# Performance work log

Hardware: AMD Instinct MI355X
Metric: run time of the kernel (lower is better)

The kernel has to match this reference:

```python
import jax, jax.numpy as jnp
import numpy as np

NUM_HEADS = 16
HEAD_DIM = 64  # att_output_dim // num_heads = 1024 // 16


def setup_inputs() -> dict:
    key = jax.random.key(0)
    ks = jax.random.split(key, 7)
    B, S, D_IN, D_OUT = 4, 2048, 1024, 1024
    std = 1.0 / np.sqrt(D_IN)
    return {
        "ts10_input": jax.random.normal(ks[0], (B, S, D_IN), dtype=jnp.float32),
        "Wq": jax.random.uniform(ks[1], (D_IN, D_OUT), jnp.float32, -std, std),
        "bq": jax.random.uniform(ks[2], (D_OUT,), jnp.float32, -std, std),
        "Wk": jax.random.uniform(ks[3], (D_IN, D_OUT), jnp.float32, -std, std),
        "bk": jax.random.uniform(ks[4], (D_OUT,), jnp.float32, -std, std),
        "Wv": jax.random.uniform(ks[5], (D_IN, D_OUT), jnp.float32, -std, std),
        "bv": jax.random.uniform(ks[6], (D_OUT,), jnp.float32, -std, std),
        "mask": 1,
    }


def reference(ts10_input, Wq, bq, Wk, bk, Wv, bv, mask):
    B, S, _ = ts10_input.shape
    H, Dh = NUM_HEADS, HEAD_DIM

    def split_heads(x):  # (B,S,H*Dh) -> (B,H,S,Dh)
        return x.reshape(B, S, H, Dh).transpose(0, 2, 1, 3)

    q = split_heads(ts10_input @ Wq + bq)
    k = split_heads(ts10_input @ Wk + bk)
    v = split_heads(ts10_input @ Wv + bv)

    scores = jnp.einsum("bhqd,bhkd->bhqk", q, k) / jnp.sqrt(jnp.float32(Dh))
    if mask:
        causal = jnp.tril(jnp.ones((S, S), dtype=bool))  # keep lower triangle incl diag
        scores = jnp.where(causal, scores, -jnp.inf)
    probs = jax.nn.softmax(scores, axis=-1)
    ctx = jnp.einsum("bhqk,bhkd->bhqd", probs, v)
    return ctx.transpose(0, 2, 1, 3).reshape(B, S, H * Dh)
```

## Files before the change

kernel.cpp:

```cpp
#include <hip/hip_runtime.h>

typedef __bf16 bf16x8 __attribute__((ext_vector_type(8)));
typedef __bf16 bf16x4 __attribute__((ext_vector_type(4)));
typedef short s16x4 __attribute__((ext_vector_type(4)));
typedef float f32x4 __attribute__((ext_vector_type(4)));
typedef unsigned short u16x8 __attribute__((ext_vector_type(8)));
typedef unsigned short u16x4 __attribute__((ext_vector_type(4)));
typedef unsigned int u32x2 __attribute__((ext_vector_type(2)));
typedef unsigned int __attribute__((address_space(1))) as1_uint;
typedef unsigned int __attribute__((address_space(3))) as3_uint;

#define S_LEN 2048
#define NB 4
#define NH 16
#define HD 64
#define DM 1024

#define Q_SCALE 0.18033688011112042f

__device__ __forceinline__ unsigned short f2bf(float f) {
  union { float f; unsigned int u; } v; v.f = f;
  unsigned int r = v.u + 0x7fffu + ((v.u >> 16) & 1u);
  return (unsigned short)(r >> 16);
}

__device__ __forceinline__ unsigned int fbits(float f) {
  union { float f; unsigned int u; } v; v.f = f;
  return v.u;
}

__device__ __forceinline__ f32x4 mfma16(u16x4 a, u16x4 b, f32x4 c) {
#if __has_builtin(__builtin_amdgcn_mfma_f32_16x16x16_bf16)
  return __builtin_amdgcn_mfma_f32_16x16x16_bf16(
      __builtin_bit_cast(bf16x4, a), __builtin_bit_cast(bf16x4, b), c, 0, 0, 0);
#else
  return __builtin_amdgcn_mfma_f32_16x16x16bf16_1k(
      __builtin_bit_cast(s16x4, a), __builtin_bit_cast(s16x4, b), c, 0, 0, 0);
#endif
}

__global__ __launch_bounds__(256) void cvt_x(const float* __restrict__ x,
                                             unsigned short* __restrict__ xb) {
  int i = (blockIdx.x * 256 + threadIdx.x) * 8;
  f32x4 a = *(const f32x4*)(x + i);
  f32x4 b = *(const f32x4*)(x + i + 4);
  u16x8 o;
  o[0] = f2bf(a[0]); o[1] = f2bf(a[1]); o[2] = f2bf(a[2]); o[3] = f2bf(a[3]);
  o[4] = f2bf(b[0]); o[5] = f2bf(b[1]); o[6] = f2bf(b[2]); o[7] = f2bf(b[3]);
  *(u16x8*)(xb + i) = o;
}

__global__ __launch_bounds__(256) void cvt_wt(const float* __restrict__ Wq,
                                              const float* __restrict__ Wk,
                                              const float* __restrict__ Wv,
                                              unsigned short* __restrict__ wt) {
  const float* W = (blockIdx.z == 0) ? Wq : (blockIdx.z == 1) ? Wk : Wv;
  unsigned short* WT = wt + (size_t)blockIdx.z * DM * DM;
  __shared__ float tile[32][33];
  int tx = threadIdx.x & 31, ty = threadIdx.x >> 5;
  int k0 = blockIdx.x * 32, n0 = blockIdx.y * 32;
#pragma unroll
  for (int i = 0; i < 4; ++i)
    tile[ty + 8 * i][tx] = W[(size_t)(k0 + ty + 8 * i) * DM + n0 + tx];
  __syncthreads();
#pragma unroll
  for (int i = 0; i < 4; ++i)
    WT[(size_t)(n0 + ty + 8 * i) * DM + k0 + tx] = f2bf(tile[tx][ty + 8 * i]);
}

__global__ __launch_bounds__(256) void qkv_gemm(const unsigned short* __restrict__ xb,
                                                const unsigned short* __restrict__ wt,
                                                const float* __restrict__ bq,
                                                const float* __restrict__ bk,
                                                const float* __restrict__ bv,
                                                unsigned short* __restrict__ qo,
                                                unsigned short* __restrict__ ko,
                                                unsigned short* __restrict__ vto) {
  const int z = blockIdx.z;
  const unsigned short* WT = wt + (size_t)z * DM * DM;
  const float* bias = (z == 0) ? bq : (z == 1) ? bk : bv;
  const int m0 = blockIdx.x * 128;
  const int n0 = blockIdx.y * 128;
  __shared__ __align__(16) unsigned short Al[128 * 32];
  __shared__ __align__(16) unsigned short Bl[128 * 32];
  const int tid = threadIdx.x;
  const int wave = tid >> 6, lane = tid & 63, quad = lane >> 4, lw = lane & 15;
  const int wm = (wave >> 1) * 64, wn = (wave & 1) * 64;

  f32x4 acc[4][4];
#pragma unroll
  for (int mt = 0; mt < 4; ++mt)
#pragma unroll
    for (int nt = 0; nt < 4; ++nt) acc[mt][nt] = (f32x4){0.f, 0.f, 0.f, 0.f};

  for (int k0 = 0; k0 < DM; k0 += 32) {
    __syncthreads();
#pragma unroll
    for (int i = 0; i < 2; ++i) {
      int c = i * 256 + tid;
      const unsigned short* ga = xb + (size_t)(m0 + (c >> 2)) * DM + k0 + (c & 3) * 8;
      __builtin_amdgcn_global_load_lds((const as1_uint*)ga, (as3_uint*)(Al + c * 8), 16, 0, 0);
      const unsigned short* gb = WT + (size_t)(n0 + (c >> 2)) * DM + k0 + (c & 3) * 8;
      __builtin_amdgcn_global_load_lds((const as1_uint*)gb, (as3_uint*)(Bl + c * 8), 16, 0, 0);
    }
    __syncthreads();
    bf16x8 af[4], bfr[4];
#pragma unroll
    for (int mt = 0; mt < 4; ++mt)
      af[mt] = *(const bf16x8*)(Al + (wm + mt * 16 + lw) * 32 + quad * 8);
#pragma unroll
    for (int nt = 0; nt < 4; ++nt)
      bfr[nt] = *(const bf16x8*)(Bl + (wn + nt * 16 + lw) * 32 + quad * 8);
#pragma unroll
    for (int mt = 0; mt < 4; ++mt)
#pragma unroll
      for (int nt = 0; nt < 4; ++nt)
        acc[mt][nt] = __builtin_amdgcn_mfma_f32_16x16x32_bf16(af[mt], bfr[nt], acc[mt][nt], 0, 0, 0);
  }

  float bias4[4];
#pragma unroll
  for (int nt = 0; nt < 4; ++nt) bias4[nt] = bias[n0 + wn + nt * 16 + lw];

  if (z < 2) {
    unsigned short* dst = (z == 0) ? qo : ko;
    const float sc = (z == 0) ? Q_SCALE : 1.0f;
#pragma unroll
    for (int mt = 0; mt < 4; ++mt) {
#pragma unroll
      for (int nt = 0; nt < 4; ++nt) {
        int n = n0 + wn + nt * 16 + lw;
        int h = n >> 6, d = n & 63;
#pragma unroll
        for (int r = 0; r < 4; ++r) {
          int m = m0 + wm + mt * 16 + quad * 4 + r;
          int b = m >> 11, s = m & 2047;
          dst[((size_t)(b * NH + h) * S_LEN + s) * HD + d] = f2bf((acc[mt][nt][r] + bias4[nt]) * sc);
        }
      }
    }
  } else {
#pragma unroll
    for (int mt = 0; mt < 4; ++mt) {
#pragma unroll
      for (int nt = 0; nt < 4; ++nt) {
        int n = n0 + wn + nt * 16 + lw;
        int h = n >> 6, d = n & 63;
        int mb = m0 + wm + mt * 16 + quad * 4;
        int b = mb >> 11, s = mb & 2047;
        u16x4 pk;
#pragma unroll
        for (int r = 0; r < 4; ++r) pk[r] = f2bf(acc[mt][nt][r] + bias4[nt]);
        *(u16x4*)(vto + ((size_t)(b * NH + h) * HD + d) * S_LEN + s) = pk;
      }
    }
  }
}

__global__ __launch_bounds__(256, 4) void attn(const unsigned short* __restrict__ Qb,
                                               const unsigned short* __restrict__ Kb,
                                               const unsigned short* __restrict__ Vtb,
                                               float* __restrict__ out) {
  const int flat = blockIdx.x;
  const int bh_lo = flat & 7;
  const int qpair = (flat >> 3) & 15;
  const int bh_hi = flat >> 7;
  const int bh = bh_lo + 8 * bh_hi;
  const int b = bh >> 4, h = bh & 15;
  const int tid = threadIdx.x;
  const int wave = tid >> 6, lane = tid & 63;
  const int quad = lane >> 4, lw = lane & 15;
  const int qlo = qpair * 64;
  const int qhi = (31 - qpair) * 64;
  const unsigned short* Qp = Qb + (size_t)bh * S_LEN * HD;
  const unsigned short* Kp = Kb + (size_t)bh * S_LEN * HD;
  const unsigned short* Vp = Vtb + (size_t)bh * HD * S_LEN;

  __shared__ __align__(16) unsigned short Kl[64 * 64];
  __shared__ __align__(16) unsigned short Vl[64 * 64];

  bf16x8 aq[2][2];
#pragma unroll
  for (int rg = 0; rg < 2; ++rg) {
    const int qbase = rg ? qhi : qlo;
#pragma unroll
    for (int kc = 0; kc < 2; ++kc)
      aq[rg][kc] = *(const bf16x8*)(Qp + (size_t)(qbase + wave * 16 + lw) * HD + kc * 32 + quad * 8);
  }

  u16x4 ones4;
#pragma unroll
  for (int i = 0; i < 4; ++i) ones4[i] = 0x3F80;

  f32x4 accO[2][4];
  f32x4 accL[2];
#pragma unroll
  for (int rg = 0; rg < 2; ++rg) {
    accL[rg] = (f32x4){0.f, 0.f, 0.f, 0.f};
#pragma unroll
    for (int dg = 0; dg < 4; ++dg) accO[rg][dg] = (f32x4){0.f, 0.f, 0.f, 0.f};
  }

  const int qr0 = qlo + wave * 16 + lw;
  const int qr1 = qhi + wave * 16 + lw;

  const int T = 32 - qpair;
  for (int t = 0; t < T; ++t) {
    const int kv = t * 64;
    __syncthreads();
#pragma unroll
    for (int i = 0; i < 2; ++i) {
      int idx = i * 256 + tid;
      int r = idx >> 3, c = (idx & 7) ^ (r & 7);
      __builtin_amdgcn_global_load_lds((const as1_uint*)(Kp + (size_t)(kv + r) * HD + c * 8),
                                       (as3_uint*)(Kl + idx * 8), 16, 0, 0);
      __builtin_amdgcn_global_load_lds((const as1_uint*)(Vp + (size_t)r * S_LEN + kv + c * 8),
                                       (as3_uint*)(Vl + idx * 8), 16, 0, 0);
    }
    __syncthreads();

    const bool a0 = (t <= qpair);
    const bool d0 = (t == qpair);
    const bool d1 = (t == T - 1);

#pragma unroll
    for (int g = 0; g < 4; ++g) {
      const unsigned short* kp = Kl + (g * 16 + lw) * 64;
      const int sw = lw & 7;
      bf16x8 kf0 = *(const bf16x8*)(kp + ((quad ^ sw) * 8));
      bf16x8 kf1 = *(const bf16x8*)(kp + (((4 + quad) ^ sw) * 8));

      u16x4 pf[2];
#pragma unroll
      for (int rg = 0; rg < 2; ++rg) {
        if (rg == 0 && !a0) continue;
        f32x4 s = (f32x4){0.f, 0.f, 0.f, 0.f};
        s = __builtin_amdgcn_mfma_f32_16x16x32_bf16(kf0, aq[rg][0], s, 0, 0, 0);
        s = __builtin_amdgcn_mfma_f32_16x16x32_bf16(kf1, aq[rg][1], s, 0, 0, 0);
        const bool dg_ = rg ? d1 : d0;
        const int qr = rg ? qr1 : qr0;
        if (dg_) {
#pragma unroll
          for (int r = 0; r < 4; ++r) {
            float e = __builtin_amdgcn_exp2f(s[r]);
            s[r] = (kv + g * 16 + quad * 4 + r > qr) ? 0.f : e;
          }
        } else {
#pragma unroll
          for (int r = 0; r < 4; ++r) s[r] = __builtin_amdgcn_exp2f(s[r]);
        }
        u32x2 pk;
        pk[0] = (fbits(s[1]) & 0xFFFF0000u) | (fbits(s[0]) >> 16);
        pk[1] = (fbits(s[3]) & 0xFFFF0000u) | (fbits(s[2]) >> 16);
        pf[rg] = __builtin_bit_cast(u16x4, pk);
      }

#pragma unroll
      for (int dg = 0; dg < 4; ++dg) {
        const int row = dg * 16 + lw;
        const int slot = (2 * g + (quad >> 1)) ^ (lw & 7);
        u16x4 vf = *(const u16x4*)(Vl + row * 64 + slot * 8 + (quad & 1) * 4);
        if (a0) accO[0][dg] = mfma16(pf[0], vf, accO[0][dg]);
        accO[1][dg] = mfma16(pf[1], vf, accO[1][dg]);
      }
      if (a0) accL[0] = mfma16(pf[0], ones4, accL[0]);
      accL[1] = mfma16(pf[1], ones4, accL[1]);
    }
  }

#pragma unroll
  for (int rg = 0; rg < 2; ++rg) {
    const int qbase = rg ? qhi : qlo;
    float* op = out + ((size_t)b * S_LEN + qbase + wave * 16 + quad * 4) * DM + h * HD + lw;
#pragma unroll
    for (int r = 0; r < 4; ++r) {
      float inv = 1.0f / accL[rg][r];
#pragma unroll
      for (int dg = 0; dg < 4; ++dg) op[(size_t)r * DM + dg * 16] = accO[rg][dg][r] * inv;
    }
  }
}

extern "C" void kernel_launch(void* const* d_in, const int* in_sizes, int n_in,
                              void* d_out, int out_size, void* d_ws, size_t ws_size,
                              hipStream_t stream) {
  const float* x = (const float*)d_in[0];
  const float* Wq = (const float*)d_in[1];
  const float* bq = (const float*)d_in[2];
  const float* Wk = (const float*)d_in[3];
  const float* bk = (const float*)d_in[4];
  const float* Wv = (const float*)d_in[5];
  const float* bv = (const float*)d_in[6];
  float* out = (float*)d_out;

  char* ws = (char*)d_ws;
  unsigned short* xb = (unsigned short*)(ws + 0);
  unsigned short* wt = (unsigned short*)(ws + 16777216);
  unsigned short* qb = (unsigned short*)(ws + 23068672);
  unsigned short* kb = (unsigned short*)(ws + 39845888);
  unsigned short* vt = (unsigned short*)(ws + 56623104);

  hipLaunchKernelGGL(cvt_x, dim3(4096), dim3(256), 0, stream, x, xb);
  hipLaunchKernelGGL(cvt_wt, dim3(32, 32, 3), dim3(256), 0, stream, Wq, Wk, Wv, wt);
  hipLaunchKernelGGL(qkv_gemm, dim3(64, 8, 3), dim3(256), 0, stream,
                     xb, wt, bq, bk, bv, qb, kb, vt);
  hipLaunchKernelGGL(attn, dim3(1024), dim3(256), 0, stream, qb, kb, vt, out);
}
```

Before: 227.9 us.

## Double-buffer K/V tiles in attention and swizzle GEMM LDS layout

The attention kernel now keeps two shared-memory buffers for the K and V tiles. It prefetches the next KV tile with async global-to-LDS loads while the MFMA work runs on the current tile, hiding global load latency behind compute. The cost is double the LDS footprint, which may reduce occupancy. Separately, the QKV projection GEMM XOR-swizzles its 16-byte chunk placement in LDS by row, to cut bank conflicts on the fragment reads.

```diff
diff --git a/kernel.cpp b/kernel.cpp
--- a/kernel.cpp
+++ b/kernel.cpp
@@ -98,19 +98,25 @@
 #pragma unroll
     for (int i = 0; i < 2; ++i) {
       int c = i * 256 + tid;
-      const unsigned short* ga = xb + (size_t)(m0 + (c >> 2)) * DM + k0 + (c & 3) * 8;
+      int row = c >> 2;
+      int scn = (c & 3) ^ ((row >> 1) & 3);
+      const unsigned short* ga = xb + (size_t)(m0 + row) * DM + k0 + scn * 8;
       __builtin_amdgcn_global_load_lds((const as1_uint*)ga, (as3_uint*)(Al + c * 8), 16, 0, 0);
-      const unsigned short* gb = WT + (size_t)(n0 + (c >> 2)) * DM + k0 + (c & 3) * 8;
+      const unsigned short* gb = WT + (size_t)(n0 + row) * DM + k0 + scn * 8;
       __builtin_amdgcn_global_load_lds((const as1_uint*)gb, (as3_uint*)(Bl + c * 8), 16, 0, 0);
     }
     __syncthreads();
     bf16x8 af[4], bfr[4];
 #pragma unroll
-    for (int mt = 0; mt < 4; ++mt)
-      af[mt] = *(const bf16x8*)(Al + (wm + mt * 16 + lw) * 32 + quad * 8);
-#pragma unroll
-    for (int nt = 0; nt < 4; ++nt)
-      bfr[nt] = *(const bf16x8*)(Bl + (wn + nt * 16 + lw) * 32 + quad * 8);
+    for (int mt = 0; mt < 4; ++mt) {
+      int r = wm + mt * 16 + lw;
+      af[mt] = *(const bf16x8*)(Al + r * 32 + (quad ^ ((r >> 1) & 3)) * 8);
+    }
+#pragma unroll
+    for (int nt = 0; nt < 4; ++nt) {
+      int r = wn + nt * 16 + lw;
+      bfr[nt] = *(const bf16x8*)(Bl + r * 32 + (quad ^ ((r >> 1) & 3)) * 8);
+    }
 #pragma unroll
     for (int mt = 0; mt < 4; ++mt)
 #pragma unroll
@@ -176,8 +182,8 @@
   const unsigned short* Kp = Kb + (size_t)bh * S_LEN * HD;
   const unsigned short* Vp = Vtb + (size_t)bh * HD * S_LEN;
 
-  __shared__ __align__(16) unsigned short Kl[64 * 64];
-  __shared__ __align__(16) unsigned short Vl[64 * 64];
+  __shared__ __align__(16) unsigned short Kl[2][64 * 64];
+  __shared__ __align__(16) unsigned short Vl[2][64 * 64];
 
   bf16x8 aq[2][2];
 #pragma unroll
@@ -205,19 +211,36 @@
   const int qr1 = qhi + wave * 16 + lw;
 
   const int T = 32 - qpair;
-  for (int t = 0; t < T; ++t) {
-    const int kv = t * 64;
-    __syncthreads();
+
+  {
 #pragma unroll
     for (int i = 0; i < 2; ++i) {
       int idx = i * 256 + tid;
       int r = idx >> 3, c = (idx & 7) ^ (r & 7);
-      __builtin_amdgcn_global_load_lds((const as1_uint*)(Kp + (size_t)(kv + r) * HD + c * 8),
-                                       (as3_uint*)(Kl + idx * 8), 16, 0, 0);
-      __builtin_amdgcn_global_load_lds((const as1_uint*)(Vp + (size_t)r * S_LEN + kv + c * 8),
-                                       (as3_uint*)(Vl + idx * 8), 16, 0, 0);
-    }
+      __builtin_amdgcn_global_load_lds((const as1_uint*)(Kp + (size_t)r * HD + c * 8),
+                                       (as3_uint*)(Kl[0] + idx * 8), 16, 0, 0);
+      __builtin_amdgcn_global_load_lds((const as1_uint*)(Vp + (size_t)r * S_LEN + c * 8),
+                                       (as3_uint*)(Vl[0] + idx * 8), 16, 0, 0);
+    }
+  }
+
+  for (int t = 0; t < T; ++t) {
+    const int kv = t * 64;
+    const int cur = t & 1;
     __syncthreads();
+
+    if (t + 1 < T) {
+      const int kvn = kv + 64;
+#pragma unroll
+      for (int i = 0; i < 2; ++i) {
+        int idx = i * 256 + tid;
+        int r = idx >> 3, c = (idx & 7) ^ (r & 7);
+        __builtin_amdgcn_global_load_lds((const as1_uint*)(Kp + (size_t)(kvn + r) * HD + c * 8),
+                                         (as3_uint*)(Kl[cur ^ 1] + idx * 8), 16, 0, 0);
+        __builtin_amdgcn_global_load_lds((const as1_uint*)(Vp + (size_t)r * S_LEN + kvn + c * 8),
+                                         (as3_uint*)(Vl[cur ^ 1] + idx * 8), 16, 0, 0);
+      }
+    }
 
     const bool a0 = (t <= qpair);
     const bool d0 = (t == qpair);
@@ -225,7 +248,7 @@
 
 #pragma unroll
     for (int g = 0; g < 4; ++g) {
-      const unsigned short* kp = Kl + (g * 16 + lw) * 64;
+      const unsigned short* kp = Kl[cur] + (g * 16 + lw) * 64;
       const int sw = lw & 7;
       bf16x8 kf0 = *(const bf16x8*)(kp + ((quad ^ sw) * 8));
       bf16x8 kf1 = *(const bf16x8*)(kp + (((4 + quad) ^ sw) * 8));
@@ -259,7 +282,7 @@
       for (int dg = 0; dg < 4; ++dg) {
         const int row = dg * 16 + lw;
         const int slot = (2 * g + (quad >> 1)) ^ (lw & 7);
-        u16x4 vf = *(const u16x4*)(Vl + row * 64 + slot * 8 + (quad & 1) * 4);
+        u16x4 vf = *(const u16x4*)(Vl[cur] + row * 64 + slot * 8 + (quad & 1) * 4);
         if (a0) accO[0][dg] = mfma16(pf[0], vf, accO[0][dg]);
         accO[1][dg] = mfma16(pf[1], vf, accO[1][dg]);
       }
```

After: 224.8 us. No clear change (-1.4%).
